# Performance work log

Measured on AMD Instinct MI355X. Metric: run time of the kernel, lower is better.

The kernel has to match this reference:

```python
import jax, jax.numpy as jnp
import numpy as np

K = 8               # config.k
X_MIN = -1.0        # x_min
X_MAX = 1.0         # x_max
GLOBAL_COEFF = 1.0  # config.global_coeff
EPS = 1e-8          # torch cosine_similarity eps
BZ, P, D = 8192, 1024, 1024  # batch, num_pool, data_dim


def setup_inputs() -> dict:
    key = jax.random.key(0)
    k1, k2, k3, k4, k5 = jax.random.split(key, 5)
    return {
        "ppg": jax.random.normal(k1, (BZ, 1, D), dtype=jnp.float32),
        "keys_pool": jax.random.normal(k2, (P, D), dtype=jnp.float32),
        "prompt_pool": jax.random.normal(k3, (P, D), dtype=jnp.float32),
        "cnn_w": jax.random.normal(k4, (1, 1, 3), dtype=jnp.float32) * 0.5,
        "cnn_b": jax.random.normal(k5, (1,), dtype=jnp.float32) * 0.1,
    }


def _prompt_cnn(prompt, w, b):
    # PromptCNN: Conv1d(1,1,k=3,pad=1) + ReLU on [P, D]
    x = prompt[:, None, :]  # [P, 1, D]
    y = jax.lax.conv_general_dilated(
        x, w, window_strides=(1,), padding=((1, 1),),
        dimension_numbers=("NCH", "OIH", "NCH"))
    y = jax.nn.relu(y + b[None, :, None])
    return y[:, 0, :]  # [P, D]


def _global_normalizer(prompt, x_min, x_max):
    pmax = jnp.max(prompt, axis=-1, keepdims=True)
    pmin = jnp.min(prompt, axis=-1, keepdims=True)
    scale = (x_max - x_min) / (pmax - pmin)
    return scale * (prompt - pmin) + x_min


def reference(ppg, keys_pool, prompt_pool, cnn_w, cnn_b):
    # prompt pool through CNN
    pcnn = _prompt_cnn(prompt_pool, cnn_w, cnn_b)  # [P, D]

    # cosine similarity: ppg [bz,1,D] vs keys [P,D] -> [bz,P]
    pn = ppg[:, 0, :] / jnp.maximum(
        jnp.linalg.norm(ppg[:, 0, :], axis=-1, keepdims=True), EPS)
    kn = keys_pool / jnp.maximum(
        jnp.linalg.norm(keys_pool, axis=-1, keepdims=True), EPS)
    cos = jnp.einsum("bd,pd->bp", pn, kn)  # [bz, P]
    score_ = 1.0 - cos

    # top-k smallest distances (largest=False) -> ascending order
    neg_vals, idx = jax.lax.top_k(-score_, K)  # [bz, K]
    score = -neg_vals

    # entropy of softmax over raw scores
    logp = jax.nn.log_softmax(score_, axis=-1)
    entropy = -(jnp.exp(logp) * logp).sum(axis=-1).mean()

    # gather selected prompts, average over k, add singleton channel dim
    prompt = pcnn[idx].mean(axis=1)[:, None, :]  # [bz, 1, D]

    # min-max global normalization (glonorm=True)
    prompt = _global_normalizer(prompt, X_MIN, X_MAX)

    # additive combine (mul=False)
    prompted = ppg + GLOBAL_COEFF * prompt  # [bz, 1, D]

    return prompted, score.mean(), entropy
```

## Files before the change

kernel.cpp:

```cpp
#include <hip/hip_runtime.h>
#include <hip/hip_bf16.h>

#define BZ 8192
#define PP 1024
#define DD 1024
#define KSEL 8

typedef unsigned short u16;
typedef unsigned long long u64;
typedef __attribute__((ext_vector_type(8))) short bf16x8;
typedef __attribute__((ext_vector_type(4))) float f32x4;

#define WS_INVK 0
#define WS_INVP 1024
#define WS_SCORE 9216
#define WS_ENT 17408
#define WS_IDX 25600
#define WS_BF16_BYTE 368640ull

__device__ __forceinline__ u16 f2bf(float x) {
  __hip_bfloat16 h = __float2bfloat16(x);
  return *(u16*)&h;
}
__device__ __forceinline__ float bf2f(u16 u) {
  __hip_bfloat16 h; *(u16*)&h = u;
  return __bfloat162float(h);
}
__device__ __forceinline__ void gll16(const void* g, void* l) {
  __builtin_amdgcn_global_load_lds((__attribute__((address_space(1))) void*)g,
                                   (__attribute__((address_space(3))) void*)l, 16, 0, 0);
}

__global__ __launch_bounds__(256) void convert_kernel(const float* __restrict__ ppg,
                                                      const float* __restrict__ keys,
                                                      float* __restrict__ ws) {
  u16* Ahi = (u16*)((char*)ws + WS_BF16_BYTE);
  u16* Alo = Ahi + 8388608;
  u16* Bhi = Alo + 8388608;
  u16* Blo = Bhi + 1048576;

  int blk = blockIdx.x;
  const float* src; u16 *hi, *lo; float* invdst;
  if (blk < PP) {
    src = keys + (size_t)blk * DD;
    hi = Bhi + (size_t)blk * DD; lo = Blo + (size_t)blk * DD;
    invdst = ws + WS_INVK + blk;
  } else {
    int r = blk - PP;
    src = ppg + (size_t)r * DD;
    hi = Ahi + (size_t)r * DD; lo = Alo + (size_t)r * DD;
    invdst = ws + WS_INVP + r;
  }
  int t = threadIdx.x;
  float4 v = ((const float4*)src)[t];
  float x[4] = {v.x, v.y, v.z, v.w};
  u16 h4[4], l4[4];
  float s = 0.f;
  #pragma unroll
  for (int j = 0; j < 4; ++j) {
    h4[j] = f2bf(x[j]);
    l4[j] = f2bf(x[j] - bf2f(h4[j]));
    s += x[j] * x[j];
  }
  *(ushort4*)(hi + t * 4) = *(ushort4*)h4;
  *(ushort4*)(lo + t * 4) = *(ushort4*)l4;

  __shared__ float red[4];
  #pragma unroll
  for (int o = 32; o > 0; o >>= 1) s += __shfl_down(s, o);
  if ((t & 63) == 0) red[t >> 6] = s;
  __syncthreads();
  if (t == 0) {
    float tot = red[0] + red[1] + red[2] + red[3];
    *invdst = 1.0f / fmaxf(sqrtf(tot), 1e-8f);
  }
}

#define LDS_AH 0
#define LDS_AL 8192
#define LDS_BH 16384
#define LDS_BL 24576

__global__ __launch_bounds__(256, 2) void gemm_mfma(const float* __restrict__ ws_ro,
                                                    float* __restrict__ C) {
  const u16* Ahi = (const u16*)((const char*)ws_ro + WS_BF16_BYTE);
  const u16* Alo = Ahi + 8388608;
  const u16* Bhi = Alo + 8388608;
  const u16* Blo = Bhi + 1048576;

  __shared__ u16 lds[32768];

  int t = threadIdx.x;
  int wid = t >> 6, lane = t & 63;
  int lr = lane & 15, lg = lane >> 4;

  int orig = blockIdx.x;
  int wg = (orig & 7) * 64 + (orig >> 3);
  int bm0 = (wg >> 3) * 128;
  int bn0 = (wg & 7) * 128;
  int wm = wid >> 1, wn = wid & 1;

  size_t offA[4], offB[4];
  int ldso[4];
  #pragma unroll
  for (int r = 0; r < 4; ++r) {
    int s = r * 256 + t;
    int row = s >> 3, g = s & 7;
    offA[r] = (size_t)(bm0 + row) * DD + g * 8;
    offB[r] = (size_t)(bn0 + row) * DD + g * 8;
    ldso[r] = (r * 256 + wid * 64) * 8;
  }

  f32x4 acc[4][4] = {};

  for (int kt = 0; kt < 16; ++kt) {
    int k0 = kt * 64;
    #pragma unroll
    for (int r = 0; r < 4; ++r) {
      gll16(Ahi + offA[r] + k0, &lds[LDS_AH + ldso[r]]);
      gll16(Alo + offA[r] + k0, &lds[LDS_AL + ldso[r]]);
      gll16(Bhi + offB[r] + k0, &lds[LDS_BH + ldso[r]]);
      gll16(Blo + offB[r] + k0, &lds[LDS_BL + ldso[r]]);
    }
    __syncthreads();

    #pragma unroll
    for (int kh = 0; kh < 2; ++kh) {
      bf16x8 ah[4], al[4], bh[4], bl[4];
      #pragma unroll
      for (int i = 0; i < 4; ++i) {
        int off = (wm * 64 + i * 16 + lr) * 64 + kh * 32 + lg * 8;
        ah[i] = *(const bf16x8*)&lds[LDS_AH + off];
        al[i] = *(const bf16x8*)&lds[LDS_AL + off];
      }
      #pragma unroll
      for (int j = 0; j < 4; ++j) {
        int off = (wn * 64 + j * 16 + lr) * 64 + kh * 32 + lg * 8;
        bh[j] = *(const bf16x8*)&lds[LDS_BH + off];
        bl[j] = *(const bf16x8*)&lds[LDS_BL + off];
      }
      #pragma unroll
      for (int i = 0; i < 4; ++i)
        #pragma unroll
        for (int j = 0; j < 4; ++j) {
          acc[i][j] = __builtin_amdgcn_mfma_f32_16x16x32_bf16(ah[i], bh[j], acc[i][j], 0, 0, 0);
          acc[i][j] = __builtin_amdgcn_mfma_f32_16x16x32_bf16(ah[i], bl[j], acc[i][j], 0, 0, 0);
          acc[i][j] = __builtin_amdgcn_mfma_f32_16x16x32_bf16(al[i], bh[j], acc[i][j], 0, 0, 0);
        }
    }
    __syncthreads();
  }

  const float* invP = ws_ro + WS_INVP;
  const float* invK = ws_ro + WS_INVK;
  #pragma unroll
  for (int i = 0; i < 4; ++i) {
    #pragma unroll
    for (int q = 0; q < 4; ++q) {
      int row = bm0 + wm * 64 + i * 16 + lg * 4 + q;
      float ip = invP[row];
      #pragma unroll
      for (int j = 0; j < 4; ++j) {
        int col = bn0 + wn * 64 + j * 16 + lr;
        C[(size_t)row * PP + col] = acc[i][j][q] * ip * invK[col];
      }
    }
  }
}

__global__ __launch_bounds__(256) void topk_wave_kernel(const float* __restrict__ cosm,
                                                        float* __restrict__ ws) {
  int wid = threadIdx.x >> 6, lane = threadIdx.x & 63;
  int row = blockIdx.x * 4 + wid;
  const float* crow = cosm + (size_t)row * PP;

  float c[16];
  #pragma unroll
  for (int p = 0; p < 4; ++p) {
    f32x4 v = *(const f32x4*)(crow + p * 256 + lane * 4);
    c[p * 4 + 0] = v[0]; c[p * 4 + 1] = v[1]; c[p * 4 + 2] = v[2]; c[p * 4 + 3] = v[3];
  }

  float z = 0.f, w = 0.f;
  #pragma unroll
  for (int l = 0; l < 16; ++l) {
    float s = 1.0f - c[l];
    float e = __expf(s - 2.0f);
    z += e; w += s * e;
  }
  #pragma unroll
  for (int o = 1; o < 64; o <<= 1) { z += __shfl_xor(z, o); w += __shfl_xor(w, o); }
  if (lane == 0) ws[WS_ENT + row] = 2.0f + __logf(z) - w / z;

  u64 k[16];
  #pragma unroll
  for (int l = 0; l < 16; ++l) {
    unsigned fb = __builtin_bit_cast(unsigned, c[l]);
    unsigned mv = fb ^ ((unsigned)((int)fb >> 31) | 0x80000000u);
    int g = ((l >> 2) << 8) | (lane << 2) | (l & 3);
    k[l] = ((u64)mv << 10) | (unsigned)(1023 - g);
  }

  float score_sum = 0.f;
  int myidx = 0;
  #pragma unroll
  for (int it = 0; it < KSEL; ++it) {
    u64 m = k[0];
    #pragma unroll
    for (int l = 1; l < 16; ++l) m = (k[l] > m) ? k[l] : m;
    #pragma unroll
    for (int o = 1; o < 64; o <<= 1) {
      u64 p = __shfl_xor(m, o);
      m = (p > m) ? p : m;
    }
    unsigned mv2 = (unsigned)(m >> 10);
    unsigned fb2 = mv2 ^ ((mv2 & 0x80000000u) ? 0x80000000u : 0xFFFFFFFFu);
    score_sum += 1.0f - __builtin_bit_cast(float, fb2);
    if (lane == it) myidx = 1023 - (int)(m & 1023u);
    #pragma unroll
    for (int l = 0; l < 16; ++l) k[l] = (k[l] == m) ? 0ull : k[l];
  }
  if (lane == 0) ws[WS_SCORE + row] = score_sum;
  if (lane < KSEL) ((int*)(ws + WS_IDX))[row * KSEL + lane] = myidx;
}

__global__ __launch_bounds__(256) void prompt_kernel(const float* __restrict__ ppg,
                                                     const float* __restrict__ pool,
                                                     const float* __restrict__ cw,
                                                     const float* __restrict__ cb,
                                                     const float* __restrict__ ws,
                                                     float* __restrict__ out) {
  int row = blockIdx.x;
  int t = threadIdx.x;
  int lane = t & 63;
  const int* idx = (const int*)(ws + WS_IDX) + row * KSEL;
  float w0 = cw[0], w1 = cw[1], w2 = cw[2], bb = cb[0];
  int d0 = t * 4;

  float a0 = 0.f, a1 = 0.f, a2 = 0.f, a3 = 0.f;
  #pragma unroll
  for (int j = 0; j < KSEL; ++j) {
    int r = idx[j];
    const float* src = pool + (size_t)r * DD;
    f32x4 x = *(const f32x4*)(src + d0);
    float xm_n = __shfl_up(x[3], 1);
    float xp_n = __shfl_down(x[0], 1);
    float xm, xp;
    if (lane == 0)  xm = (t > 0)   ? src[d0 - 1] : 0.f;
    else            xm = xm_n;
    if (lane == 63) xp = (t < 255) ? src[d0 + 4] : 0.f;
    else            xp = xp_n;
    float y0 = fmaf(w0, xm,   fmaf(w1, x[0], fmaf(w2, x[1], bb)));
    float y1 = fmaf(w0, x[0], fmaf(w1, x[1], fmaf(w2, x[2], bb)));
    float y2 = fmaf(w0, x[1], fmaf(w1, x[2], fmaf(w2, x[3], bb)));
    float y3 = fmaf(w0, x[2], fmaf(w1, x[3], fmaf(w2, xp,   bb)));
    a0 += fmaxf(y0, 0.f);
    a1 += fmaxf(y1, 0.f);
    a2 += fmaxf(y2, 0.f);
    a3 += fmaxf(y3, 0.f);
  }
  a0 *= 0.125f; a1 *= 0.125f; a2 *= 0.125f; a3 *= 0.125f;

  __shared__ float rmin[4], rmax[4];
  float lmin = fminf(fminf(a0, a1), fminf(a2, a3));
  float lmax = fmaxf(fmaxf(a0, a1), fmaxf(a2, a3));
  #pragma unroll
  for (int o = 32; o > 0; o >>= 1) {
    lmin = fminf(lmin, __shfl_down(lmin, o));
    lmax = fmaxf(lmax, __shfl_down(lmax, o));
  }
  if ((t & 63) == 0) { rmin[t >> 6] = lmin; rmax[t >> 6] = lmax; }
  __syncthreads();
  float pmin = fminf(fminf(rmin[0], rmin[1]), fminf(rmin[2], rmin[3]));
  float pmax = fmaxf(fmaxf(rmax[0], rmax[1]), fmaxf(rmax[2], rmax[3]));
  float scale = 2.0f / (pmax - pmin);

  f32x4 pv = *(const f32x4*)(ppg + (size_t)row * DD + d0);
  f32x4 o4;
  o4[0] = pv[0] + (scale * (a0 - pmin) - 1.0f);
  o4[1] = pv[1] + (scale * (a1 - pmin) - 1.0f);
  o4[2] = pv[2] + (scale * (a2 - pmin) - 1.0f);
  o4[3] = pv[3] + (scale * (a3 - pmin) - 1.0f);
  *(f32x4*)(out + (size_t)row * DD + d0) = o4;
}

__global__ __launch_bounds__(256) void finalize_kernel(const float* __restrict__ ws,
                                                       float* __restrict__ out) {
  int t = threadIdx.x;
  const float* ss = ws + WS_SCORE;
  const float* ee = ws + WS_ENT;
  float s = 0.f, e = 0.f;
  for (int i = t; i < BZ; i += 256) { s += ss[i]; e += ee[i]; }
  __shared__ float rs[4], re[4];
  #pragma unroll
  for (int o = 32; o > 0; o >>= 1) { s += __shfl_down(s, o); e += __shfl_down(e, o); }
  if ((t & 63) == 0) { rs[t >> 6] = s; re[t >> 6] = e; }
  __syncthreads();
  if (t == 0) {
    float sT = rs[0] + rs[1] + rs[2] + rs[3];
    float eT = re[0] + re[1] + re[2] + re[3];
    out[(size_t)BZ * DD + 0] = sT / (float)(BZ * KSEL);
    out[(size_t)BZ * DD + 1] = eT / (float)BZ;
  }
}

extern "C" void kernel_launch(void* const* d_in, const int* in_sizes, int n_in,
                              void* d_out, int out_size, void* d_ws, size_t ws_size,
                              hipStream_t stream) {
  const float* ppg  = (const float*)d_in[0];
  const float* keys = (const float*)d_in[1];
  const float* pool = (const float*)d_in[2];
  const float* cw   = (const float*)d_in[3];
  const float* cb   = (const float*)d_in[4];
  float* out = (float*)d_out;
  float* ws  = (float*)d_ws;

  hipLaunchKernelGGL(convert_kernel, dim3(PP + BZ), dim3(256), 0, stream, ppg, keys, ws);
  hipLaunchKernelGGL(gemm_mfma, dim3((BZ / 128) * (PP / 128)), dim3(256), 0, stream, ws, out);
  hipLaunchKernelGGL(topk_wave_kernel, dim3(BZ / 4), dim3(256), 0, stream, out, ws);
  hipLaunchKernelGGL(prompt_kernel, dim3(BZ), dim3(256), 0, stream, ppg, pool, cw, cb, ws, out);
  hipLaunchKernelGGL(finalize_kernel, dim3(1), dim3(256), 0, stream, ws, out);
}
```

Baseline: 125.7 us.

## Precompute prompt CNN once per pool row and halve GEMM K-tile for occupancy

Adds a kernel that applies the conv+ReLU to each of the 1024 prompt-pool rows once and stores the result in workspace, so the per-batch prompt kernel only gathers and averages precomputed rows instead of redoing the conv 8 times per batch row. Separately, the MFMA GEMM K tile shrinks from 64 to 32, halving LDS use and raising launch bounds to 4 blocks per CU. The trade-offs are an extra launch, a 4 MB workspace buffer, and twice as many K-loop barriers in the GEMM.

```diff
diff --git a/kernel.cpp b/kernel.cpp
--- a/kernel.cpp
+++ b/kernel.cpp
@@ -17,6 +17,7 @@
 #define WS_ENT 17408
 #define WS_IDX 25600
 #define WS_BF16_BYTE 368640ull
+#define WS_PCNN_BYTE 38117376ull
 
 __device__ __forceinline__ u16 f2bf(float x) {
   __hip_bfloat16 h = __float2bfloat16(x);
@@ -76,19 +77,45 @@
   }
 }
 
+__global__ __launch_bounds__(256) void pcnn_kernel(const float* __restrict__ pool,
+                                                   const float* __restrict__ cw,
+                                                   const float* __restrict__ cb,
+                                                   float* __restrict__ ws) {
+  float* pcnn = (float*)((char*)ws + WS_PCNN_BYTE);
+  int row = blockIdx.x;
+  int t = threadIdx.x;
+  int d0 = t * 4;
+  const float* src = pool + (size_t)row * DD;
+  float w0 = cw[0], w1 = cw[1], w2 = cw[2], bb = cb[0];
+
+  f32x4 x = *(const f32x4*)(src + d0);
+  float xm = (d0 > 0) ? src[d0 - 1] : 0.f;
+  float xp = (d0 + 4 < DD) ? src[d0 + 4] : 0.f;
+  float y0 = fmaf(w0, xm,   fmaf(w1, x[0], fmaf(w2, x[1], bb)));
+  float y1 = fmaf(w0, x[0], fmaf(w1, x[1], fmaf(w2, x[2], bb)));
+  float y2 = fmaf(w0, x[1], fmaf(w1, x[2], fmaf(w2, x[3], bb)));
+  float y3 = fmaf(w0, x[2], fmaf(w1, x[3], fmaf(w2, xp,   bb)));
+  f32x4 o4;
+  o4[0] = fmaxf(y0, 0.f);
+  o4[1] = fmaxf(y1, 0.f);
+  o4[2] = fmaxf(y2, 0.f);
+  o4[3] = fmaxf(y3, 0.f);
+  *(f32x4*)(pcnn + (size_t)row * DD + d0) = o4;
+}
+
 #define LDS_AH 0
-#define LDS_AL 8192
-#define LDS_BH 16384
-#define LDS_BL 24576
-
-__global__ __launch_bounds__(256, 2) void gemm_mfma(const float* __restrict__ ws_ro,
+#define LDS_AL 4096
+#define LDS_BH 8192
+#define LDS_BL 12288
+
+__global__ __launch_bounds__(256, 4) void gemm_mfma(const float* __restrict__ ws_ro,
                                                     float* __restrict__ C) {
   const u16* Ahi = (const u16*)((const char*)ws_ro + WS_BF16_BYTE);
   const u16* Alo = Ahi + 8388608;
   const u16* Bhi = Alo + 8388608;
   const u16* Blo = Bhi + 1048576;
 
-  __shared__ u16 lds[32768];
+  __shared__ u16 lds[16384];
 
   int t = threadIdx.x;
   int wid = t >> 6, lane = t & 63;
@@ -100,12 +127,12 @@
   int bn0 = (wg & 7) * 128;
   int wm = wid >> 1, wn = wid & 1;
 
-  size_t offA[4], offB[4];
-  int ldso[4];
-  #pragma unroll
-  for (int r = 0; r < 4; ++r) {
+  size_t offA[2], offB[2];
+  int ldso[2];
+  #pragma unroll
+  for (int r = 0; r < 2; ++r) {
     int s = r * 256 + t;
-    int row = s >> 3, g = s & 7;
+    int row = s >> 2, g = s & 3;
     offA[r] = (size_t)(bm0 + row) * DD + g * 8;
     offB[r] = (size_t)(bn0 + row) * DD + g * 8;
     ldso[r] = (r * 256 + wid * 64) * 8;
@@ -113,10 +140,10 @@
 
   f32x4 acc[4][4] = {};
 
-  for (int kt = 0; kt < 16; ++kt) {
-    int k0 = kt * 64;
-    #pragma unroll
-    for (int r = 0; r < 4; ++r) {
+  for (int kt = 0; kt < 32; ++kt) {
+    int k0 = kt * 32;
+    #pragma unroll
+    for (int r = 0; r < 2; ++r) {
       gll16(Ahi + offA[r] + k0, &lds[LDS_AH + ldso[r]]);
       gll16(Alo + offA[r] + k0, &lds[LDS_AL + ldso[r]]);
       gll16(Bhi + offB[r] + k0, &lds[LDS_BH + ldso[r]]);
@@ -124,30 +151,27 @@
     }
     __syncthreads();
 
-    #pragma unroll
-    for (int kh = 0; kh < 2; ++kh) {
-      bf16x8 ah[4], al[4], bh[4], bl[4];
-      #pragma unroll
-      for (int i = 0; i < 4; ++i) {
-        int off = (wm * 64 + i * 16 + lr) * 64 + kh * 32 + lg * 8;
-        ah[i] = *(const bf16x8*)&lds[LDS_AH + off];
-        al[i] = *(const bf16x8*)&lds[LDS_AL + off];
-      }
+    bf16x8 ah[4], al[4], bh[4], bl[4];
+    #pragma unroll
+    for (int i = 0; i < 4; ++i) {
+      int off = (wm * 64 + i * 16 + lr) * 32 + lg * 8;
+      ah[i] = *(const bf16x8*)&lds[LDS_AH + off];
+      al[i] = *(const bf16x8*)&lds[LDS_AL + off];
+    }
+    #pragma unroll
+    for (int j = 0; j < 4; ++j) {
+      int off = (wn * 64 + j * 16 + lr) * 32 + lg * 8;
+      bh[j] = *(const bf16x8*)&lds[LDS_BH + off];
+      bl[j] = *(const bf16x8*)&lds[LDS_BL + off];
+    }
+    #pragma unroll
+    for (int i = 0; i < 4; ++i)
       #pragma unroll
       for (int j = 0; j < 4; ++j) {
-        int off = (wn * 64 + j * 16 + lr) * 64 + kh * 32 + lg * 8;
-        bh[j] = *(const bf16x8*)&lds[LDS_BH + off];
-        bl[j] = *(const bf16x8*)&lds[LDS_BL + off];
+        acc[i][j] = __builtin_amdgcn_mfma_f32_16x16x32_bf16(ah[i], bh[j], acc[i][j], 0, 0, 0);
+        acc[i][j] = __builtin_amdgcn_mfma_f32_16x16x32_bf16(ah[i], bl[j], acc[i][j], 0, 0, 0);
+        acc[i][j] = __builtin_amdgcn_mfma_f32_16x16x32_bf16(al[i], bh[j], acc[i][j], 0, 0, 0);
       }
-      #pragma unroll
-      for (int i = 0; i < 4; ++i)
-        #pragma unroll
-        for (int j = 0; j < 4; ++j) {
-          acc[i][j] = __builtin_amdgcn_mfma_f32_16x16x32_bf16(ah[i], bh[j], acc[i][j], 0, 0, 0);
-          acc[i][j] = __builtin_amdgcn_mfma_f32_16x16x32_bf16(ah[i], bl[j], acc[i][j], 0, 0, 0);
-          acc[i][j] = __builtin_amdgcn_mfma_f32_16x16x32_bf16(al[i], bh[j], acc[i][j], 0, 0, 0);
-        }
-    }
     __syncthreads();
   }
 
@@ -225,39 +249,21 @@
 }
 
 __global__ __launch_bounds__(256) void prompt_kernel(const float* __restrict__ ppg,
-                                                     const float* __restrict__ pool,
-                                                     const float* __restrict__ cw,
-                                                     const float* __restrict__ cb,
+                                                     const float* __restrict__ ws_ro,
                                                      const float* __restrict__ ws,
                                                      float* __restrict__ out) {
+  const float* pcnn = (const float*)((const char*)ws_ro + WS_PCNN_BYTE);
   int row = blockIdx.x;
   int t = threadIdx.x;
-  int lane = t & 63;
   const int* idx = (const int*)(ws + WS_IDX) + row * KSEL;
-  float w0 = cw[0], w1 = cw[1], w2 = cw[2], bb = cb[0];
   int d0 = t * 4;
 
   float a0 = 0.f, a1 = 0.f, a2 = 0.f, a3 = 0.f;
   #pragma unroll
   for (int j = 0; j < KSEL; ++j) {
     int r = idx[j];
-    const float* src = pool + (size_t)r * DD;
-    f32x4 x = *(const f32x4*)(src + d0);
-    float xm_n = __shfl_up(x[3], 1);
-    float xp_n = __shfl_down(x[0], 1);
-    float xm, xp;
-    if (lane == 0)  xm = (t > 0)   ? src[d0 - 1] : 0.f;
-    else            xm = xm_n;
-    if (lane == 63) xp = (t < 255) ? src[d0 + 4] : 0.f;
-    else            xp = xp_n;
-    float y0 = fmaf(w0, xm,   fmaf(w1, x[0], fmaf(w2, x[1], bb)));
-    float y1 = fmaf(w0, x[0], fmaf(w1, x[1], fmaf(w2, x[2], bb)));
-    float y2 = fmaf(w0, x[1], fmaf(w1, x[2], fmaf(w2, x[3], bb)));
-    float y3 = fmaf(w0, x[2], fmaf(w1, x[3], fmaf(w2, xp,   bb)));
-    a0 += fmaxf(y0, 0.f);
-    a1 += fmaxf(y1, 0.f);
-    a2 += fmaxf(y2, 0.f);
-    a3 += fmaxf(y3, 0.f);
+    f32x4 x = *(const f32x4*)(pcnn + (size_t)r * DD + d0);
+    a0 += x[0]; a1 += x[1]; a2 += x[2]; a3 += x[3];
   }
   a0 *= 0.125f; a1 *= 0.125f; a2 *= 0.125f; a3 *= 0.125f;
 
@@ -316,8 +322,9 @@
   float* ws  = (float*)d_ws;
 
   hipLaunchKernelGGL(convert_kernel, dim3(PP + BZ), dim3(256), 0, stream, ppg, keys, ws);
+  hipLaunchKernelGGL(pcnn_kernel, dim3(PP), dim3(256), 0, stream, pool, cw, cb, ws);
   hipLaunchKernelGGL(gemm_mfma, dim3((BZ / 128) * (PP / 128)), dim3(256), 0, stream, ws, out);
   hipLaunchKernelGGL(topk_wave_kernel, dim3(BZ / 4), dim3(256), 0, stream, out, ws);
-  hipLaunchKernelGGL(prompt_kernel, dim3(BZ), dim3(256), 0, stream, ppg, pool, cw, cb, ws, out);
+  hipLaunchKernelGGL(prompt_kernel, dim3(BZ), dim3(256), 0, stream, ppg, ws, ws, out);
   hipLaunchKernelGGL(finalize_kernel, dim3(1), dim3(256), 0, stream, ws, out);
 }
```

Result: no change. 126.9 us (+1.0%).
